# Kernel tuning notes

Hardware: AMD Instinct MI355X
Metric: run time of the kernel (lower is better)

## Reference

```python
import jax, jax.numpy as jnp
from jax import lax
import numpy as np

K = 5  # length_inter_tile
EPS = 0.01


def _conv(x, w, b):
    y = lax.conv_general_dilated(x, w, (1, 1), ((1, 1), (1, 1)),
                                 dimension_numbers=('NCHW', 'OIHW', 'NCHW'))
    return y + b[None, :, None, None]


def _leaky(x):
    return jnp.where(x >= 0, x, 0.01 * x)


def _unfold(x, k=K):
    # torch F.unfold(x, k, padding=k//2): (b,c,h,w) -> (b, c*k*k, h*w), channel-major ordering
    b, c, h, w = x.shape
    p = k // 2
    xp = jnp.pad(x, ((0, 0), (0, 0), (p, p), (p, p)))
    pat = jnp.stack([xp[:, :, i:i + h, j:j + w] for i in range(k) for j in range(k)], axis=2)
    return pat.reshape(b, c * k * k, h * w)


def _fold(x, c, h, w, k=K):
    # torch F.fold: (b, c*k*k, h*w) -> (b, c, h, w) with overlap-add, padding=k//2
    b = x.shape[0]
    p = k // 2
    xr = x.reshape(b, c, k, k, h, w)
    out = jnp.zeros((b, c, h + 2 * p, w + 2 * p), x.dtype)
    for i in range(k):
        for j in range(k):
            out = out.at[:, :, i:i + h, j:j + w].add(xr[:, :, i, j])
    return out[:, :, p:p + h, p:p + w]


def _mmn(x, axes):
    mn = jnp.min(x, axis=axes, keepdims=True)
    mx = jnp.max(x, axis=axes, keepdims=True)
    return (x - mn) / (mx - mn + 0.001)


def setup_inputs() -> dict:
    key = jax.random.key(0)
    ks = jax.random.split(key, 8)
    b, t, ch_in, h, w = 1, 16, 10, 24, 24
    t_de, ch_de = 16, 12
    sc = 0.02
    return {
        'x': jax.random.normal(ks[0], (b, t, ch_in, h, w), jnp.float32),
        'design': jax.random.uniform(ks[1], (b, t_de, ch_de, h, w), jnp.float32),
        'gt': jax.random.uniform(ks[2], (b, t_de, 3, h, w), jnp.float32),
        'w1': jax.random.normal(ks[3], (1024, 160, 3, 3), jnp.float32) * sc,
        'b1': jnp.zeros((1024,), jnp.float32),
        'w2': jax.random.normal(ks[4], (1024, 1024, 3, 3), jnp.float32) * sc,
        'b2': jnp.zeros((1024,), jnp.float32),
        'w3': jax.random.normal(ks[5], (1024, 1024, 3, 3), jnp.float32) * sc,
        'b3': jnp.zeros((1024,), jnp.float32),
        'wf': jax.random.normal(ks[6], (6400, 1024, 3, 3), jnp.float32) * sc,
        'bf': jnp.zeros((6400,), jnp.float32),
    }


def _forward(x, design, gt, w1, b1, w2, b2, w3, b3, wf, bf):
    b, t, ch_in, h, w = x.shape
    t_de, ch_de = design.shape[1], design.shape[2]
    hw = h * w
    N = K * K  # num_inter

    # unfold design: (b, t_de*ch_de*N, hw) -> (b*hw, N, t_de, ch_de)
    d = _unfold(design.reshape(b, t_de * ch_de, h, w))
    d = d.transpose(0, 2, 1).reshape(b * hw, t_de * ch_de, N)
    d = d.transpose(0, 2, 1).reshape(b * hw, N, t_de, ch_de)

    # norm in each prediction window (per channel-group, per sample)
    d = jnp.concatenate([
        d[..., 0:1],
        _mmn(d[..., 1:4], (1, 2, 3)),
        _mmn(d[..., 4:5], (1, 2)),
        _mmn(d[..., 5:8], (1, 2, 3)),
        _mmn(d[..., 8:], (1, 2)),  # each grid channel independently
    ], axis=-1)

    M = b * hw * N
    domain = d.reshape(M, t_de, ch_de)
    X = d[:, :, :t, :].reshape(M, t, ch_de)

    # feature network (n_layers=4 -> 3 leaky convs) + weight head
    f = _leaky(_conv(x.reshape(b, t * ch_in, h, w), w1, b1))
    f = _leaky(_conv(f, w2, b2))
    f = _leaky(_conv(f, w3, b3))
    Wt = jnp.tanh(_conv(f, wf, bf))  # (b, N*t*t, h, w)
    Wm = Wt.reshape(b, N, t, t, h, w).transpose(0, 4, 5, 1, 2, 3).reshape(M, t, t)
    Wm = jnp.einsum('nij,nkj->nik', Wm, Wm) + jnp.eye(t, dtype=Wm.dtype)

    XTW = jnp.einsum('ntc,ntu->ncu', X, Wm)          # (M, ch_de, t)
    XTWX = jnp.einsum('nct,ntd->ncd', XTW, X)        # (M, ch_de, ch_de)
    A = XTWX.reshape(b * hw, N, ch_de, ch_de).sum(1) + EPS * jnp.eye(ch_de, dtype=XTWX.dtype)

    # reference for loss (unfolded)
    ref = _unfold(gt.reshape(b, t_de * 3, h, w))
    ref = ref.transpose(0, 2, 1).reshape(b * hw, t_de * 3, N)
    ref = ref.transpose(0, 2, 1).reshape(M, t_de, 3)

    outs, folded = [], []
    for ch in range(3):
        Y = _unfold(x[:, :, ch])                      # (b, t*N, hw)
        Y = Y.transpose(0, 2, 1).reshape(b * hw, t, N)
        Y = Y.transpose(0, 2, 1).reshape(M, t, 1)
        XTWY = jnp.einsum('nct,nto->nco', XTW, Y)
        Bv = XTWY.reshape(b * hw, N, ch_de, 1).sum(1)
        para = jnp.linalg.solve(A, Bv)                # (b*hw, ch_de, 1)
        para_r = jnp.broadcast_to(para[:, None], (b * hw, N, ch_de, 1)).reshape(M, ch_de, 1)
        o = jnp.einsum('ntc,nco->nto', domain, para_r)  # (M, t_de, 1)
        outs.append(o[..., 0])
        # overlap-add fold of per-window predictions
        oc = o.reshape(b, hw, N, t_de).transpose(0, 3, 2, 1).reshape(b, t_de * N, hw)
        num = _fold(oc, t_de, h, w)
        den = _fold(jnp.ones_like(oc), t_de, h, w)
        folded.append(num / den)

    out_for_loss = jnp.stack(outs, axis=-1)           # (M, t_de, 3)
    out = jnp.stack(folded, axis=2)                   # (b, t_de, 3, h, w)
    loss = jnp.mean(jnp.abs(out_for_loss - ref))      # L1 stand-in for loss_for_stit_v1
    return out, loss


def reference(x, design, gt, w1, b1, w2, b2, w3, b3, wf, bf):
    return _forward(x, design, gt, w1, b1, w2, b2, w3, b3, wf, bf)
```

## Files before the change

### kernel.cpp

```cpp
#include <hip/hip_runtime.h>
#include <math.h>


typedef __attribute__((ext_vector_type(8))) short sh8;
typedef __attribute__((ext_vector_type(4))) float f32x4;

#define OFF_PART 0UL
#define OFF_X2T  58982400UL
#define OFF_WTT  58982400UL
#define OFF_ACT  85524480UL
#define OFF_DN   87883776UL
#define OFF_OB   98942976UL
#define OFF_MN   101707776UL
#define OFF_MX   101723904UL
#define OFF_LP   101740032UL


__device__ inline void glds16(const void* gsrc, void* ldst) {
    __builtin_amdgcn_global_load_lds((const __attribute__((address_space(1))) void*)gsrc,
                                     (__attribute__((address_space(3))) void*)ldst, 16, 0, 0);
}

__global__ __launch_bounds__(64) void minmax_kernel(const float* __restrict__ design,
                                                    float* __restrict__ mn_o,
                                                    float* __restrict__ mx_o) {
    int p = blockIdx.x;
    int py = p / 24, px = p % 24;
    int lane = threadIdx.x;
    float mn[7], mx[7];
#pragma unroll
    for (int g = 0; g < 7; g++) { mn[g] = 1e30f; mx[g] = -1e30f; }
    for (int e = lane; e < 400; e += 64) {
        int n = e / 16, td = e % 16;
        int yy = py + n / 5 - 2, xx = px + n % 5 - 2;
        bool ok = (yy >= 0 && yy < 24 && xx >= 0 && xx < 24);
#pragma unroll
        for (int cd = 1; cd < 12; cd++) {
            float v = ok ? design[(td * 12 + cd) * 576 + yy * 24 + xx] : 0.0f;
            int g = (cd <= 3) ? 0 : (cd == 4) ? 1 : (cd <= 7) ? 2 : 3 + (cd - 8);
            mn[g] = fminf(mn[g], v);
            mx[g] = fmaxf(mx[g], v);
        }
    }
#pragma unroll
    for (int s = 32; s >= 1; s >>= 1) {
#pragma unroll
        for (int g = 0; g < 7; g++) {
            mn[g] = fminf(mn[g], __shfl_xor(mn[g], s));
            mx[g] = fmaxf(mx[g], __shfl_xor(mx[g], s));
        }
    }
    if (lane == 0) {
#pragma unroll
        for (int g = 0; g < 7; g++) {
            mn_o[p * 7 + g] = mn[g];
            mx_o[p * 7 + g] = mx[g];
        }
    }
}

__global__ void dnorm_kernel(const float* __restrict__ design,
                             const float* __restrict__ mn,
                             const float* __restrict__ mx,
                             float* __restrict__ dn) {
    int idx = blockIdx.x * 256 + threadIdx.x;
    if (idx >= 14400 * 192) return;
    int cd = idx % 12;
    int td = (idx / 12) % 16;
    int n  = (idx / 192) % 25;
    int p  = idx / 4800;
    int py = p / 24, px = p % 24;
    int yy = py + n / 5 - 2, xx = px + n % 5 - 2;
    float v = (yy >= 0 && yy < 24 && xx >= 0 && xx < 24)
                  ? design[(td * 12 + cd) * 576 + yy * 24 + xx] : 0.0f;
    if (cd >= 1) {
        int g = (cd <= 3) ? 0 : (cd == 4) ? 1 : (cd <= 7) ? 2 : 3 + (cd - 8);
        float a = mn[p * 7 + g], b = mx[p * 7 + g];
        v = (v - a) / (b - a + 0.001f);
    }
    dn[idx] = v;
}

__global__ __launch_bounds__(256) void im2col_kernel(const float* __restrict__ act,
                                                     char* __restrict__ x2t, int nrows) {
    int row = blockIdx.x * 256 + threadIdx.x;
    if (row >= nrows) return;
    int kc = row / 576, px = row % 576;
    int y = px / 24, x = px % 24;
    int k0 = kc * 32;
    int ic = k0 / 9;
    int tap = k0 - ic * 9;
    sh8 hv[4], lv[4];
#pragma unroll
    for (int e = 0; e < 32; ++e) {
        int dy = tap / 3, dx = tap - dy * 3;
        int yy = y + dy - 1, xx = x + dx - 1;
        float v = (yy >= 0 && yy < 24 && xx >= 0 && xx < 24)
                      ? act[ic * 576 + yy * 24 + xx] : 0.0f;
        unsigned u = __builtin_bit_cast(unsigned, v);
        hv[e / 8][e % 8] = (short)(u >> 16);
        float fh = __builtin_bit_cast(float, u & 0xFFFF0000u);
        lv[e / 8][e % 8] = (short)(__builtin_bit_cast(unsigned, v - fh) >> 16);
        if (++tap == 9) { tap = 0; ++ic; }
    }
    char* dst = x2t + (long)kc * 92160 + (long)px * 80;
#pragma unroll
    for (int s4 = 0; s4 < 4; ++s4) {
        *(sh8*)(dst + s4 * 16) = hv[s4];
        *(sh8*)(dst + 46080 + s4 * 16) = lv[s4];
    }
}

__global__ void finalize_kernel(const float* __restrict__ part,
                                const float* __restrict__ bias,
                                float* __restrict__ act, int total, int nsplit) {
    int idx = blockIdx.x * 256 + threadIdx.x;
    if (idx >= total) return;
    float s = 0.0f;
    for (int k = 0; k < nsplit; k++) s += part[(long)k * total + idx];
    s += bias[idx / 576];
    act[idx] = s >= 0.0f ? s : 0.01f * s;
}

template<int SWZ>
__global__ __launch_bounds__(256, 2)
void conv_mfma4_kernel(const char* __restrict__ x2t,
                       const float* __restrict__ wgt,
                       float* __restrict__ part,
                       int K, int cps, int cout) {
    __shared__ __align__(1024) char sA[2][16384];
    __shared__ __align__(1024) char sB[46080];

    const int tid = threadIdx.x;
    const int lane = tid & 63;
    const int w = tid >> 6;
    const int wo = w >> 1, wp = w & 1;
    const int q = lane >> 4, ln15 = lane & 15;

    int ocb, pxh, s;
    if (SWZ) {
        int g = blockIdx.x;
        int xcd = g & 7, slot = g >> 3;
        int p = xcd + 8 * (slot >> 1);
        ocb = p % 50; s = p / 50; pxh = slot & 1;
    } else {
        ocb = blockIdx.x; pxh = blockIdx.y; s = blockIdx.z;
    }
    const long K4 = (long)K * 4;
    const int c0 = s * cps;

    const int arow = lane >> 3;
    const int acol = (lane & 7) * 16;
    const int sw = (ln15 & 7) << 4;
    const int bbase = (wp * 144 + ln15) * 80 + q * 16;

    f32x4 acc[4][9];
#pragma unroll
    for (int a = 0; a < 4; ++a)
#pragma unroll
        for (int j = 0; j < 9; ++j) acc[a][j] = f32x4{0.f, 0.f, 0.f, 0.f};

    const char* wsrc0 = (const char*)wgt + (long)(ocb * 128) * K4;

    {
        const char* wsrc = wsrc0 + (long)c0 * 128;
        for (int it = w; it < 16; it += 4) {
            int r = it * 8 + arow;
            glds16(wsrc + (long)r * K4 + (acol ^ ((r & 7) << 4)), sA[0] + it * 1024);
        }
    }

#pragma unroll 1
    for (int t = 0; t < cps; ++t) {
        const int cc = c0 + t;
        __syncthreads();
        {
            const char* bsrc = x2t + (long)cc * 92160 + pxh * 23040;
            for (int it = w; it < 45; it += 4) {
                int boff = it * 1024 + lane * 16;
                const char* src = (boff < 23040) ? bsrc + boff
                                                 : bsrc + 46080 + (boff - 23040);
                glds16(src, sB + it * 1024);
            }
        }
        if (t + 1 < cps) {
            const char* wsrc = wsrc0 + (long)(cc + 1) * 128;
            char* dst = sA[(t + 1) & 1];
            for (int it = w; it < 16; it += 4) {
                int r = it * 8 + arow;
                glds16(wsrc + (long)r * K4 + (acol ^ ((r & 7) << 4)), dst + it * 1024);
            }
            asm volatile("s_waitcnt vmcnt(4)" ::: "memory");
        } else {
            asm volatile("s_waitcnt vmcnt(0)" ::: "memory");
        }
        __syncthreads();

        const char* sAc = sA[t & 1];
        sh8 ah[4], al[4];
#pragma unroll
        for (int ot = 0; ot < 4; ++ot) {
            const char* ap = sAc + (wo * 64 + ot * 16 + ln15) * 128;
            float4 a0 = *(const float4*)(ap + ((q * 32) ^ sw));
            float4 a1 = *(const float4*)(ap + ((q * 32 + 16) ^ sw));
            float av[8] = {a0.x, a0.y, a0.z, a0.w, a1.x, a1.y, a1.z, a1.w};
#pragma unroll
            for (int e = 0; e < 8; ++e) {
                unsigned u = __builtin_bit_cast(unsigned, av[e]);
                ah[ot][e] = (short)(u >> 16);
                float fh = __builtin_bit_cast(float, u & 0xFFFF0000u);
                al[ot][e] = (short)(__builtin_bit_cast(unsigned, av[e] - fh) >> 16);
            }
        }
        __builtin_amdgcn_s_setprio(1);
#pragma unroll
        for (int j = 0; j < 9; ++j) {
            int ba = bbase + j * (16 * 80);
            sh8 bh = *(const sh8*)(sB + ba);
            sh8 bl = *(const sh8*)(sB + 23040 + ba);
#pragma unroll
            for (int ot = 0; ot < 4; ++ot) {
                acc[ot][j] = __builtin_amdgcn_mfma_f32_16x16x32_bf16(ah[ot], bh, acc[ot][j], 0, 0, 0);
                acc[ot][j] = __builtin_amdgcn_mfma_f32_16x16x32_bf16(al[ot], bh, acc[ot][j], 0, 0, 0);
                acc[ot][j] = __builtin_amdgcn_mfma_f32_16x16x32_bf16(ah[ot], bl, acc[ot][j], 0, 0, 0);
            }
        }
        __builtin_amdgcn_s_setprio(0);
    }
#pragma unroll
    for (int ot = 0; ot < 4; ++ot) {
        int oc0 = ocb * 128 + wo * 64 + ot * 16 + q * 4;
#pragma unroll
        for (int j = 0; j < 9; ++j) {
            int px = pxh * 288 + wp * 144 + j * 16 + ln15;
#pragma unroll
            for (int vr = 0; vr < 4; ++vr)
                part[((long)s * cout + oc0 + vr) * 576 + px] = acc[ot][j][vr];
        }
    }
}

__global__ __launch_bounds__(256) void tanh_tr_kernel(const float* __restrict__ part,
                                                      const float* __restrict__ bias,
                                                      float* __restrict__ wtT) {
    __shared__ float tile[64][65];
    int oc0 = blockIdx.x * 64, p0 = blockIdx.y * 64;
    int tx = threadIdx.x, ty = threadIdx.y;
#pragma unroll
    for (int k = 0; k < 16; k++) {
        int row = ty + k * 4;
        float s = 0.f;
#pragma unroll
        for (int sp = 0; sp < 4; ++sp)
            s += part[((long)sp * 6400 + oc0 + row) * 576 + p0 + tx];
        tile[row][tx] = tanhf(s + bias[oc0 + row]);
    }
    __syncthreads();
#pragma unroll
    for (int k = 0; k < 16; k++) {
        int rr = ty + k * 4;
        wtT[(long)(p0 + rr) * 6400 + oc0 + tx] = tile[tx][rr];
    }
}

__global__ __launch_bounds__(256) void stagec_kernel(const float* __restrict__ dn,
                                                     const float* __restrict__ wtT,
                                                     const float* __restrict__ xin,
                                                     const float* __restrict__ gt,
                                                     float* __restrict__ ob,
                                                     float* __restrict__ lp) {
    int p = blockIdx.x;
    int py = p / 24, px = p % 24;
    int tid = threadIdx.x;
    __shared__ float sX[4800];
    __shared__ float sW[6400];
    __shared__ float sY[1200];
    __shared__ float sP[192];
    __shared__ float sXTW[192];
    __shared__ float sA[144];
    __shared__ float sB[36];
    __shared__ double dA[144];
    __shared__ double db[36];
    __shared__ float spara[36];
    __shared__ float sred[256];

    for (int e = tid; e < 4800; e += 256) sX[e] = dn[(long)p * 4800 + e];
    for (int e = tid; e < 6400; e += 256) sW[e] = wtT[(long)p * 6400 + e];
    for (int e = tid; e < 1200; e += 256) {
        int n = e / 48, t = (e % 48) / 3, ch = e % 3;
        int yy = py + n / 5 - 2, xx = px + n % 5 - 2;
        sY[e] = (yy >= 0 && yy < 24 && xx >= 0 && xx < 24)
                    ? xin[(t * 10 + ch) * 576 + yy * 24 + xx] : 0.0f;
    }
    if (tid < 144) sA[tid] = 0.0f;
    if (tid < 36) sB[tid] = 0.0f;
    __syncthreads();

    for (int n = 0; n < 25; n++) {
        const float* X = sX + n * 192;
        const float* W = sW + n * 256;
        if (tid < 192) {
            int c = tid >> 4, j = tid & 15;
            float s = 0.0f;
#pragma unroll
            for (int t = 0; t < 16; t++) s = fmaf(X[t * 12 + c], W[t * 16 + j], s);
            sP[tid] = s;
        }
        __syncthreads();
        if (tid < 192) {
            int c = tid >> 4, u = tid & 15;
            float s = X[u * 12 + c];
#pragma unroll
            for (int j = 0; j < 16; j++) s = fmaf(sP[c * 16 + j], W[u * 16 + j], s);
            sXTW[tid] = s;
        }
        __syncthreads();
        if (tid < 144) {
            int c = tid / 12, d2 = tid % 12;
            float s = 0.0f;
#pragma unroll
            for (int t = 0; t < 16; t++) s = fmaf(sXTW[c * 16 + t], X[t * 12 + d2], s);
            sA[tid] += s;
        } else if (tid < 180) {
            int e = tid - 144;
            int c = e / 3, ch = e % 3;
            float s = 0.0f;
#pragma unroll
            for (int t = 0; t < 16; t++) s = fmaf(sXTW[c * 16 + t], sY[n * 48 + t * 3 + ch], s);
            sB[e] += s;
        }
        __syncthreads();
    }

    if (tid < 144) dA[tid] = (double)sA[tid] + ((tid % 13 == 0) ? 0.01 : 0.0);
    if (tid < 36) db[tid] = (double)sB[tid];
    __syncthreads();

    if (tid == 0) {
        for (int kk = 0; kk < 12; kk++) {
            double d = dA[kk * 12 + kk];
            for (int q2 = 0; q2 < kk; q2++) d -= dA[kk * 12 + q2] * dA[kk * 12 + q2];
            d = sqrt(d);
            dA[kk * 12 + kk] = d;
            double inv = 1.0 / d;
            for (int i = kk + 1; i < 12; i++) {
                double s = dA[i * 12 + kk];
                for (int q2 = 0; q2 < kk; q2++) s -= dA[i * 12 + q2] * dA[kk * 12 + q2];
                dA[i * 12 + kk] = s * inv;
            }
        }
        for (int ch = 0; ch < 3; ch++) {
            double t2[12];
            for (int i = 0; i < 12; i++) {
                double s = db[i * 3 + ch];
                for (int q2 = 0; q2 < i; q2++) s -= dA[i * 12 + q2] * t2[q2];
                t2[i] = s / dA[i * 12 + i];
            }
            for (int i = 11; i >= 0; i--) {
                double s = t2[i];
                for (int q2 = i + 1; q2 < 12; q2++) s -= dA[q2 * 12 + i] * t2[q2];
                t2[i] = s / dA[i * 12 + i];
            }
            for (int i = 0; i < 12; i++) spara[i * 3 + ch] = (float)t2[i];
        }
    }
    __syncthreads();

    float lsum = 0.0f;
    for (int e = tid; e < 1200; e += 256) {
        int n = e / 48, td = (e % 48) / 3, ch = e % 3;
        float s = 0.0f;
#pragma unroll
        for (int c = 0; c < 12; c++) s = fmaf(sX[n * 192 + td * 12 + c], spara[c * 3 + ch], s);
        ob[((long)(p * 25 + n)) * 48 + td * 3 + ch] = s;
        int yy = py + n / 5 - 2, xx = px + n % 5 - 2;
        float rv = (yy >= 0 && yy < 24 && xx >= 0 && xx < 24)
                       ? gt[(td * 3 + ch) * 576 + yy * 24 + xx] : 0.0f;
        lsum += fabsf(s - rv);
    }
    sred[tid] = lsum;
    __syncthreads();
    for (int s = 128; s >= 1; s >>= 1) {
        if (tid < s) sred[tid] += sred[tid + s];
        __syncthreads();
    }
    if (tid == 0) lp[p] = sred[0];
}

__global__ void fold_kernel(const float* __restrict__ ob, float* __restrict__ out) {
    int idx = blockIdx.x * 256 + threadIdx.x;
    if (idx >= 27648) return;
    int td = idx / 1728;
    int rem = idx % 1728;
    int ch = rem / 576;
    int p = rem % 576;
    int y = p / 24, x = p % 24;
    float num = 0.0f;
    int den = 0;
    for (int i = 0; i < 5; i++) {
        int yy = y + 2 - i;
        if (yy < 0 || yy >= 24) continue;
        for (int j = 0; j < 5; j++) {
            int xx = x + 2 - j;
            if (xx < 0 || xx >= 24) continue;
            num += ob[((long)((yy * 24 + xx) * 25 + i * 5 + j)) * 48 + td * 3 + ch];
            den++;
        }
    }
    out[idx] = num / (float)den;
}

__global__ __launch_bounds__(64) void loss_kernel(const float* __restrict__ lp,
                                                  float* __restrict__ out) {
    int t = threadIdx.x;
    float s = 0.0f;
    for (int e = t; e < 576; e += 64) s += lp[e];
#pragma unroll
    for (int d = 32; d >= 1; d >>= 1) s += __shfl_xor(s, d);
    if (t == 0) out[27648] = s / 691200.0f;
}

extern "C" void kernel_launch(void* const* d_in, const int* in_sizes, int n_in,
                              void* d_out, int out_size, void* d_ws, size_t ws_size,
                              hipStream_t stream) {
    const float* x      = (const float*)d_in[0];
    const float* design = (const float*)d_in[1];
    const float* gt     = (const float*)d_in[2];
    const float* w1     = (const float*)d_in[3];
    const float* b1     = (const float*)d_in[4];
    const float* w2     = (const float*)d_in[5];
    const float* b2     = (const float*)d_in[6];
    const float* w3     = (const float*)d_in[7];
    const float* b3     = (const float*)d_in[8];
    const float* wf     = (const float*)d_in[9];
    const float* bf     = (const float*)d_in[10];
    float* out = (float*)d_out;
    char* wsb  = (char*)d_ws;

    float* part = (float*)(wsb + OFF_PART);
    char*  x2t  = wsb + OFF_X2T;
    float* wtT  = (float*)(wsb + OFF_WTT);
    float* act  = (float*)(wsb + OFF_ACT);
    float* dn   = (float*)(wsb + OFF_DN);
    float* ob   = (float*)(wsb + OFF_OB);
    float* mn   = (float*)(wsb + OFF_MN);
    float* mx   = (float*)(wsb + OFF_MX);
    float* lp   = (float*)(wsb + OFF_LP);

    minmax_kernel<<<576, 64, 0, stream>>>(design, mn, mx);
    dnorm_kernel<<<10800, 256, 0, stream>>>(design, mn, mx, dn);

    im2col_kernel<<<102, 256, 0, stream>>>(x, x2t, 45 * 576);
    conv_mfma4_kernel<0><<<dim3(8, 2, 15), 256, 0, stream>>>(x2t, w1, part, 1440, 3, 1024);
    finalize_kernel<<<2304, 256, 0, stream>>>(part, b1, act, 589824, 15);
    im2col_kernel<<<648, 256, 0, stream>>>(act, x2t, 288 * 576);
    conv_mfma4_kernel<0><<<dim3(8, 2, 16), 256, 0, stream>>>(x2t, w2, part, 9216, 18, 1024);
    finalize_kernel<<<2304, 256, 0, stream>>>(part, b2, act, 589824, 16);
    im2col_kernel<<<648, 256, 0, stream>>>(act, x2t, 288 * 576);
    conv_mfma4_kernel<0><<<dim3(8, 2, 16), 256, 0, stream>>>(x2t, w3, part, 9216, 18, 1024);
    finalize_kernel<<<2304, 256, 0, stream>>>(part, b3, act, 589824, 16);
    im2col_kernel<<<648, 256, 0, stream>>>(act, x2t, 288 * 576);
    conv_mfma4_kernel<1><<<400, 256, 0, stream>>>(x2t, wf, part, 9216, 72, 6400);
    tanh_tr_kernel<<<dim3(100, 9), dim3(64, 4), 0, stream>>>(part, bf, wtT);

    stagec_kernel<<<576, 256, 0, stream>>>(dn, wtT, x, gt, ob, lp);
    fold_kernel<<<108, 256, 0, stream>>>(ob, out);
    loss_kernel<<<1, 64, 0, stream>>>(lp, out);
}
```

Before: 570.5 us.

## Pre-split weights to bf16 hi/lo once per tile and widen split-K

The conv kernel now loads each weight chunk into registers, converts it to bf16 high/low halves once per block, and stores the split form into LDS after the MFMA loop. Previously every wave converted the fp32 weights on each LDS read, and four waves shared the same rows, so the conversion was repeated. The global loads for the next chunk are issued before the MFMAs so their latency overlaps compute. When the workspace is large enough, conv2 and conv3 also use twice as many K splits, which adds parallelism but means writing and reducing more partial sums.

```diff
diff --git a/kernel.cpp b/kernel.cpp
--- a/kernel.cpp
+++ b/kernel.cpp
@@ -4,16 +4,6 @@
 
 typedef __attribute__((ext_vector_type(8))) short sh8;
 typedef __attribute__((ext_vector_type(4))) float f32x4;
-
-#define OFF_PART 0UL
-#define OFF_X2T  58982400UL
-#define OFF_WTT  58982400UL
-#define OFF_ACT  85524480UL
-#define OFF_DN   87883776UL
-#define OFF_OB   98942976UL
-#define OFF_MN   101707776UL
-#define OFF_MX   101723904UL
-#define OFF_LP   101740032UL
 
 
 __device__ inline void glds16(const void* gsrc, void* ldst) {
@@ -124,12 +114,12 @@
 
 template<int SWZ>
 __global__ __launch_bounds__(256, 2)
-void conv_mfma4_kernel(const char* __restrict__ x2t,
+void conv_mfma5_kernel(const char* __restrict__ x2t,
                        const float* __restrict__ wgt,
                        float* __restrict__ part,
                        int K, int cps, int cout) {
+    __shared__ __align__(1024) char sB[46080];
     __shared__ __align__(1024) char sA[2][16384];
-    __shared__ __align__(1024) char sB[46080];
 
     const int tid = threadIdx.x;
     const int lane = tid & 63;
@@ -146,12 +136,21 @@
     } else {
         ocb = blockIdx.x; pxh = blockIdx.y; s = blockIdx.z;
     }
-    const long K4 = (long)K * 4;
     const int c0 = s * cps;
 
-    const int arow = lane >> 3;
-    const int acol = (lane & 7) * 16;
-    const int sw = (ln15 & 7) << 4;
+    const int st_oc = tid >> 1;
+    const int st_h  = tid & 1;
+    const float* wrow = wgt + (long)(ocb * 128 + st_oc) * K + st_h * 16;
+    const int wslot0 = (((st_h * 2 + 0) + (st_oc >> 1)) & 3) << 4;
+    const int wslot1 = (((st_h * 2 + 1) + (st_oc >> 1)) & 3) << 4;
+    char* const arow_base = (char*)nullptr;
+
+    int aoff[4];
+#pragma unroll
+    for (int ot = 0; ot < 4; ++ot) {
+        int oc = wo * 64 + ot * 16 + ln15;
+        aoff[ot] = oc * 64 + (((q + (oc >> 1)) & 3) << 4);
+    }
     const int bbase = (wp * 144 + ln15) * 80 + q * 16;
 
     f32x4 acc[4][9];
@@ -160,14 +159,27 @@
 #pragma unroll
         for (int j = 0; j < 9; ++j) acc[a][j] = f32x4{0.f, 0.f, 0.f, 0.f};
 
-    const char* wsrc0 = (const char*)wgt + (long)(ocb * 128) * K4;
-
     {
-        const char* wsrc = wsrc0 + (long)c0 * 128;
-        for (int it = w; it < 16; it += 4) {
-            int r = it * 8 + arow;
-            glds16(wsrc + (long)r * K4 + (acol ^ ((r & 7) << 4)), sA[0] + it * 1024);
-        }
+        const float* p = wrow + (long)c0 * 32;
+        float4 a0 = *(const float4*)(p);
+        float4 a1 = *(const float4*)(p + 4);
+        float4 a2 = *(const float4*)(p + 8);
+        float4 a3 = *(const float4*)(p + 12);
+        float av[16] = {a0.x, a0.y, a0.z, a0.w, a1.x, a1.y, a1.z, a1.w,
+                        a2.x, a2.y, a2.z, a2.w, a3.x, a3.y, a3.z, a3.w};
+        sh8 h8[2], l8[2];
+#pragma unroll
+        for (int e = 0; e < 16; ++e) {
+            unsigned u = __builtin_bit_cast(unsigned, av[e]);
+            h8[e / 8][e % 8] = (short)(u >> 16);
+            float fh = __builtin_bit_cast(float, u & 0xFFFF0000u);
+            l8[e / 8][e % 8] = (short)(__builtin_bit_cast(unsigned, av[e] - fh) >> 16);
+        }
+        char* hb = sA[0] + st_oc * 64;
+        *(sh8*)(hb + wslot0) = h8[0];
+        *(sh8*)(hb + wslot1) = h8[1];
+        *(sh8*)(hb + 8192 + wslot0) = l8[0];
+        *(sh8*)(hb + 8192 + wslot1) = l8[1];
     }
 
 #pragma unroll 1
@@ -183,13 +195,15 @@
                 glds16(src, sB + it * 1024);
             }
         }
-        if (t + 1 < cps) {
-            const char* wsrc = wsrc0 + (long)(cc + 1) * 128;
-            char* dst = sA[(t + 1) & 1];
-            for (int it = w; it < 16; it += 4) {
-                int r = it * 8 + arow;
-                glds16(wsrc + (long)r * K4 + (acol ^ ((r & 7) << 4)), dst + it * 1024);
-            }
+        __builtin_amdgcn_sched_barrier(0);
+        const bool pf = (t + 1 < cps);
+        float4 a0, a1, a2, a3;
+        if (pf) {
+            const float* p = wrow + (long)(cc + 1) * 32;
+            a0 = *(const float4*)(p);
+            a1 = *(const float4*)(p + 4);
+            a2 = *(const float4*)(p + 8);
+            a3 = *(const float4*)(p + 12);
             asm volatile("s_waitcnt vmcnt(4)" ::: "memory");
         } else {
             asm volatile("s_waitcnt vmcnt(0)" ::: "memory");
@@ -200,19 +214,9 @@
         sh8 ah[4], al[4];
 #pragma unroll
         for (int ot = 0; ot < 4; ++ot) {
-            const char* ap = sAc + (wo * 64 + ot * 16 + ln15) * 128;
-            float4 a0 = *(const float4*)(ap + ((q * 32) ^ sw));
-            float4 a1 = *(const float4*)(ap + ((q * 32 + 16) ^ sw));
-            float av[8] = {a0.x, a0.y, a0.z, a0.w, a1.x, a1.y, a1.z, a1.w};
-#pragma unroll
-            for (int e = 0; e < 8; ++e) {
-                unsigned u = __builtin_bit_cast(unsigned, av[e]);
-                ah[ot][e] = (short)(u >> 16);
-                float fh = __builtin_bit_cast(float, u & 0xFFFF0000u);
-                al[ot][e] = (short)(__builtin_bit_cast(unsigned, av[e] - fh) >> 16);
-            }
-        }
-        __builtin_amdgcn_s_setprio(1);
+            ah[ot] = *(const sh8*)(sAc + aoff[ot]);
+            al[ot] = *(const sh8*)(sAc + 8192 + aoff[ot]);
+        }
 #pragma unroll
         for (int j = 0; j < 9; ++j) {
             int ba = bbase + j * (16 * 80);
@@ -225,7 +229,23 @@
                 acc[ot][j] = __builtin_amdgcn_mfma_f32_16x16x32_bf16(ah[ot], bl, acc[ot][j], 0, 0, 0);
             }
         }
-        __builtin_amdgcn_s_setprio(0);
+        if (pf) {
+            float av[16] = {a0.x, a0.y, a0.z, a0.w, a1.x, a1.y, a1.z, a1.w,
+                            a2.x, a2.y, a2.z, a2.w, a3.x, a3.y, a3.z, a3.w};
+            sh8 h8[2], l8[2];
+#pragma unroll
+            for (int e = 0; e < 16; ++e) {
+                unsigned u = __builtin_bit_cast(unsigned, av[e]);
+                h8[e / 8][e % 8] = (short)(u >> 16);
+                float fh = __builtin_bit_cast(float, u & 0xFFFF0000u);
+                l8[e / 8][e % 8] = (short)(__builtin_bit_cast(unsigned, av[e] - fh) >> 16);
+            }
+            char* hb = sA[(t + 1) & 1] + st_oc * 64;
+            *(sh8*)(hb + wslot0) = h8[0];
+            *(sh8*)(hb + wslot1) = h8[1];
+            *(sh8*)(hb + 8192 + wslot0) = l8[0];
+            *(sh8*)(hb + 8192 + wslot1) = l8[1];
+        }
     }
 #pragma unroll
     for (int ot = 0; ot < 4; ++ot) {
@@ -437,30 +457,41 @@
     float* out = (float*)d_out;
     char* wsb  = (char*)d_ws;
 
-    float* part = (float*)(wsb + OFF_PART);
-    char*  x2t  = wsb + OFF_X2T;
-    float* wtT  = (float*)(wsb + OFF_WTT);
-    float* act  = (float*)(wsb + OFF_ACT);
-    float* dn   = (float*)(wsb + OFF_DN);
-    float* ob   = (float*)(wsb + OFF_OB);
-    float* mn   = (float*)(wsb + OFF_MN);
-    float* mx   = (float*)(wsb + OFF_MX);
-    float* lp   = (float*)(wsb + OFF_LP);
+    const int big = (ws_size >= 118257408UL) ? 1 : 0;
+    const int ks23 = big ? 32 : 16;
+    const int cps23 = big ? 9 : 18;
+    size_t off_x2t = big ? 75497472UL : 58982400UL;
+    size_t off_act = off_x2t + 26542080UL;
+    size_t off_dn  = off_act + 2359296UL;
+    size_t off_ob  = off_dn + 11059200UL;
+    size_t off_mn  = off_ob + 2764800UL;
+    size_t off_mx  = off_mn + 16128UL;
+    size_t off_lp  = off_mx + 16128UL;
+
+    float* part = (float*)(wsb);
+    char*  x2t  = wsb + off_x2t;
+    float* wtT  = (float*)(wsb + off_x2t);
+    float* act  = (float*)(wsb + off_act);
+    float* dn   = (float*)(wsb + off_dn);
+    float* ob   = (float*)(wsb + off_ob);
+    float* mn   = (float*)(wsb + off_mn);
+    float* mx   = (float*)(wsb + off_mx);
+    float* lp   = (float*)(wsb + off_lp);
 
     minmax_kernel<<<576, 64, 0, stream>>>(design, mn, mx);
     dnorm_kernel<<<10800, 256, 0, stream>>>(design, mn, mx, dn);
 
     im2col_kernel<<<102, 256, 0, stream>>>(x, x2t, 45 * 576);
-    conv_mfma4_kernel<0><<<dim3(8, 2, 15), 256, 0, stream>>>(x2t, w1, part, 1440, 3, 1024);
+    conv_mfma5_kernel<0><<<dim3(8, 2, 15), 256, 0, stream>>>(x2t, w1, part, 1440, 3, 1024);
     finalize_kernel<<<2304, 256, 0, stream>>>(part, b1, act, 589824, 15);
     im2col_kernel<<<648, 256, 0, stream>>>(act, x2t, 288 * 576);
-    conv_mfma4_kernel<0><<<dim3(8, 2, 16), 256, 0, stream>>>(x2t, w2, part, 9216, 18, 1024);
-    finalize_kernel<<<2304, 256, 0, stream>>>(part, b2, act, 589824, 16);
+    conv_mfma5_kernel<0><<<dim3(8, 2, ks23), 256, 0, stream>>>(x2t, w2, part, 9216, cps23, 1024);
+    finalize_kernel<<<2304, 256, 0, stream>>>(part, b2, act, 589824, ks23);
     im2col_kernel<<<648, 256, 0, stream>>>(act, x2t, 288 * 576);
-    conv_mfma4_kernel<0><<<dim3(8, 2, 16), 256, 0, stream>>>(x2t, w3, part, 9216, 18, 1024);
-    finalize_kernel<<<2304, 256, 0, stream>>>(part, b3, act, 589824, 16);
+    conv_mfma5_kernel<0><<<dim3(8, 2, ks23), 256, 0, stream>>>(x2t, w3, part, 9216, cps23, 1024);
+    finalize_kernel<<<2304, 256, 0, stream>>>(part, b3, act, 589824, ks23);
     im2col_kernel<<<648, 256, 0, stream>>>(act, x2t, 288 * 576);
-    conv_mfma4_kernel<1><<<400, 256, 0, stream>>>(x2t, wf, part, 9216, 72, 6400);
+    conv_mfma5_kernel<1><<<400, 256, 0, stream>>>(x2t, wf, part, 9216, 72, 6400);
     tanh_tr_kernel<<<dim3(100, 9), dim3(64, 4), 0, stream>>>(part, bf, wtT);
 
     stagec_kernel<<<576, 256, 0, stream>>>(dn, wtT, x, gt, ob, lp);
```

Result: no change. 581.5 us (+1.9%).
